# Kernel optimization log

Measured on AMD Instinct MI355X. Metric: run time of the kernel, lower is better.

## Reference

```python
import jax, jax.numpy as jnp
import numpy as np
import math

D_MODEL = 1024
NHEAD = 16
SEQ_LEN = 4096
K_PROJ = 16
HEAD_DIM = D_MODEL // NHEAD


def setup_inputs() -> dict:
    key = jax.random.key(0)
    ks = jax.random.split(key, 11)
    x = jax.random.normal(ks[0], (4, SEQ_LEN, D_MODEL), dtype=jnp.float32)
    s = 1.0 / math.sqrt(D_MODEL)
    Wq = jax.random.uniform(ks[1], (D_MODEL, D_MODEL), minval=-s, maxval=s)
    bq = jax.random.uniform(ks[2], (D_MODEL,), minval=-s, maxval=s)
    Wk = jax.random.uniform(ks[3], (D_MODEL, D_MODEL), minval=-s, maxval=s)
    bk = jax.random.uniform(ks[4], (D_MODEL,), minval=-s, maxval=s)
    Wv = jax.random.uniform(ks[5], (D_MODEL, D_MODEL), minval=-s, maxval=s)
    bv = jax.random.uniform(ks[6], (D_MODEL,), minval=-s, maxval=s)
    Wo = jax.random.uniform(ks[7], (D_MODEL, D_MODEL), minval=-s, maxval=s)
    bo = jax.random.uniform(ks[8], (D_MODEL,), minval=-s, maxval=s)
    E = jax.random.normal(ks[9], (NHEAD, K_PROJ, SEQ_LEN)) * 0.02
    F = jax.random.normal(ks[10], (NHEAD, K_PROJ, SEQ_LEN)) * 0.02
    return {"x": x, "Wq": Wq, "bq": bq, "Wk": Wk, "bk": bk,
            "Wv": Wv, "bv": bv, "Wo": Wo, "bo": bo, "E": E, "F": F}


def reference(x, Wq, bq, Wk, bk, Wv, bv, Wo, bo, E, F):
    B, N, D = x.shape
    # torch Linear: y = x @ W.T + b
    q = x @ Wq.T + bq
    k = x @ Wk.T + bk
    v = x @ Wv.T + bv
    # [B, H, N, Dh]
    def split_heads(t):
        return t.reshape(B, N, NHEAD, HEAD_DIM).transpose(0, 2, 1, 3)
    q, k, v = split_heads(q), split_heads(k), split_heads(v)
    # low-rank projections of K, V along sequence: [B, H, Kp, Dh]
    k_lin = jnp.einsum('bhnd,hkn->bhkd', k, E)
    v_lin = jnp.einsum('bhnd,hkn->bhkd', v, F)
    scores = jnp.einsum('bhnd,bhkd->bhnk', q, k_lin) / math.sqrt(HEAD_DIM)
    attn = jax.nn.softmax(scores, axis=-1)  # dropout is identity in eval
    out = jnp.einsum('bhnk,bhkd->bhnd', attn, v_lin)
    out = out.transpose(0, 2, 1, 3).reshape(B, N, D)
    return out @ Wo.T + bo
```

## Files before the change

### kernel.cpp

```cpp
#include <hip/hip_runtime.h>
#include <hip/hip_bf16.h>

#define SEQLEN 4096

typedef __bf16 bf16x8 __attribute__((ext_vector_type(8)));
typedef float f32x4 __attribute__((ext_vector_type(4)));
typedef __attribute__((ext_vector_type(8))) unsigned short u16x8;

__device__ inline float bf2f(unsigned short s) {
  union { unsigned u; float f; } t; t.u = ((unsigned)s) << 16; return t.f;
}
__device__ inline unsigned short f2bf(float f) {
  __hip_bfloat16 h = __float2bfloat16(f);
  return *reinterpret_cast<unsigned short*>(&h);
}

__device__ inline void gload_lds16(const void* g, void* l) {
  __builtin_amdgcn_global_load_lds(
      (const __attribute__((address_space(1))) unsigned int*)g,
      (__attribute__((address_space(3))) unsigned int*)l, 16, 0, 0);
}

__global__ void cvt_f32_to_bf16(const float* __restrict__ s,
                                unsigned short* __restrict__ d, int n4) {
  int i = blockIdx.x * 256 + threadIdx.x;
  if (i >= n4) return;
  float4 v = reinterpret_cast<const float4*>(s)[i];
  ushort4 o;
  o.x = f2bf(v.x); o.y = f2bf(v.y); o.z = f2bf(v.z); o.w = f2bf(v.w);
  reinterpret_cast<ushort4*>(d)[i] = o;
}

__global__ void pack_bias(const float* __restrict__ a, const float* __restrict__ b,
                          const float* __restrict__ c, float* __restrict__ dst) {
  int i = blockIdx.x * 256 + threadIdx.x;
  if (i < 1024) { dst[i] = a[i]; dst[1024 + i] = b[i]; dst[2048 + i] = c[i]; }
}

template <typename OUT_T>
__global__ void gemm_bt(const unsigned short* __restrict__ A,
                        const unsigned short* __restrict__ B,
                        const float* __restrict__ bias, OUT_T* __restrict__ C,
                        int M, int N, int K, int ldc) {
  __shared__ __align__(16) unsigned short As[128 * 64];
  __shared__ __align__(16) unsigned short Bs[128 * 64];
  const int tid = threadIdx.x;
  const int lane = tid & 63, wv = tid >> 6;
  const int wr = wv >> 1, wc = wv & 1;
  const int r16 = lane & 15, kg = lane >> 4;
  const int brow = blockIdx.y * 128, bcol = blockIdx.x * 128;

  f32x4 acc[4][4];
#pragma unroll
  for (int m = 0; m < 4; ++m)
#pragma unroll
    for (int n = 0; n < 4; ++n) acc[m][n] = (f32x4)0.0f;

  for (int k0 = 0; k0 < K; k0 += 64) {
#pragma unroll
    for (int it = 0; it < 4; ++it) {
      int f = it * 256 + tid;
      int row = f >> 3, ch = f & 7;
      const unsigned short* ga = A + (size_t)(brow + row) * K + k0 + ch * 8;
      const unsigned short* gb = B + (size_t)(bcol + row) * K + k0 + ch * 8;
      gload_lds16(ga, &As[f * 8]);
      gload_lds16(gb, &Bs[f * 8]);
    }
    __syncthreads();
#pragma unroll
    for (int ks = 0; ks < 2; ++ks) {
      bf16x8 a[4], b[4];
#pragma unroll
      for (int m = 0; m < 4; ++m)
        a[m] = *reinterpret_cast<const bf16x8*>(
            &As[(wr * 64 + m * 16 + r16) * 64 + ks * 32 + kg * 8]);
#pragma unroll
      for (int n = 0; n < 4; ++n)
        b[n] = *reinterpret_cast<const bf16x8*>(
            &Bs[(wc * 64 + n * 16 + r16) * 64 + ks * 32 + kg * 8]);
#pragma unroll
      for (int m = 0; m < 4; ++m)
#pragma unroll
        for (int n = 0; n < 4; ++n)
          acc[m][n] =
              __builtin_amdgcn_mfma_f32_16x16x32_bf16(a[m], b[n], acc[m][n], 0, 0, 0);
    }
    __syncthreads();
  }

#pragma unroll
  for (int n = 0; n < 4; ++n) {
    int col = bcol + wc * 64 + n * 16 + r16;
    float bv = bias ? bias[col] : 0.0f;
#pragma unroll
    for (int m = 0; m < 4; ++m) {
#pragma unroll
      for (int r = 0; r < 4; ++r) {
        int row = brow + wr * 64 + m * 16 + kg * 4 + r;
        float v = acc[m][n][r] + bv;
        if constexpr (sizeof(OUT_T) == 2) {
          C[(size_t)row * ldc + col] = f2bf(v);
        } else {
          C[(size_t)row * ldc + col] = v;
        }
      }
    }
  }
}

__global__ void kvlin_part(const unsigned short* __restrict__ qkv,
                           const float* __restrict__ E, const float* __restrict__ F,
                           float* __restrict__ part) {
  __shared__ __align__(16) unsigned short Ks[128 * 64], Vs[128 * 64];
  __shared__ __align__(16) float Es[16 * 128], Fs[16 * 128];
  const int tid = threadIdx.x;
  const int bid = blockIdx.x;
  const int bh = bid >> 3, ns = bid & 7;
  const int b = bh >> 4, h = bh & 15;
  const int d = tid & 63, kk = tid >> 6;
  float aK[4] = {0, 0, 0, 0}, aV[4] = {0, 0, 0, 0};
  for (int c = 0; c < 4; ++c) {
    int n0 = ns * 512 + c * 128;
#pragma unroll
    for (int it = 0; it < 4; ++it) {
      int f = it * 256 + tid;
      int row = f >> 3, ch = f & 7;
      const unsigned short* gk =
          qkv + (size_t)(b * SEQLEN + n0 + row) * 3072 + 1024 + h * 64 + ch * 8;
      gload_lds16(gk, &Ks[f * 8]);
      gload_lds16(gk + 1024, &Vs[f * 8]);
    }
#pragma unroll
    for (int it = 0; it < 2; ++it) {
      int f = it * 256 + tid;
      int k = f >> 5, ch = f & 31;
      const float* ge = E + (size_t)(h * 16 + k) * SEQLEN + n0 + ch * 4;
      const float* gf = F + (size_t)(h * 16 + k) * SEQLEN + n0 + ch * 4;
      gload_lds16(ge, &Es[f * 4]);
      gload_lds16(gf, &Fs[f * 4]);
    }
    __syncthreads();
    for (int n = 0; n < 128; ++n) {
      float kv = bf2f(Ks[n * 64 + d]);
      float vv = bf2f(Vs[n * 64 + d]);
#pragma unroll
      for (int j = 0; j < 4; ++j) {
        aK[j] += Es[(kk * 4 + j) * 128 + n] * kv;
        aV[j] += Fs[(kk * 4 + j) * 128 + n] * vv;
      }
    }
    __syncthreads();
  }
  size_t base = ((size_t)ns * 64 + bh) * 2048;
#pragma unroll
  for (int j = 0; j < 4; ++j) {
    part[base + (kk * 4 + j) * 64 + d] = aK[j];
    part[base + 1024 + (kk * 4 + j) * 64 + d] = aV[j];
  }
}

__global__ void kvlin_reduce(const float* __restrict__ part, float* __restrict__ out) {
  int i = blockIdx.x * 256 + threadIdx.x;
  float s = 0;
#pragma unroll
  for (int ns = 0; ns < 8; ++ns) s += part[(size_t)ns * 131072 + i];
  out[i] = s;
}

__global__ void attn_kernel(const unsigned short* __restrict__ qkv,
                            const float* __restrict__ kvlin,
                            unsigned short* __restrict__ aout) {
  __shared__ float kl[1024], vl[1024];
  const int tid = threadIdx.x;
  const int bid = blockIdx.x;
  const int bh = bid >> 4, nt = bid & 15;
  const int b = bh >> 4, h = bh & 15;
  for (int i = tid; i < 1024; i += 256) {
    kl[i] = kvlin[(size_t)bh * 2048 + i];
    vl[i] = kvlin[(size_t)bh * 2048 + 1024 + i];
  }
  __syncthreads();
  const int n = nt * 256 + tid;
  const unsigned short* qp = qkv + (size_t)(b * SEQLEN + n) * 3072 + h * 64;
  float q[64];
#pragma unroll
  for (int c2 = 0; c2 < 8; ++c2) {
    u16x8 v = *reinterpret_cast<const u16x8*>(qp + c2 * 8);
#pragma unroll
    for (int j = 0; j < 8; ++j) q[c2 * 8 + j] = bf2f(v[j]);
  }
  float s[16];
#pragma unroll
  for (int k = 0; k < 16; ++k) {
    float a = 0;
#pragma unroll
    for (int dd = 0; dd < 64; ++dd) a += q[dd] * kl[k * 64 + dd];
    s[k] = a * 0.125f;
  }
  float mx = s[0];
#pragma unroll
  for (int k = 1; k < 16; ++k) mx = fmaxf(mx, s[k]);
  float sum = 0;
#pragma unroll
  for (int k = 0; k < 16; ++k) { s[k] = __expf(s[k] - mx); sum += s[k]; }
  float inv = 1.0f / sum;
#pragma unroll
  for (int k = 0; k < 16; ++k) s[k] *= inv;
  unsigned short* op = aout + (size_t)(b * SEQLEN + n) * 1024 + h * 64;
#pragma unroll
  for (int d0 = 0; d0 < 8; ++d0) {
    float o[8] = {0, 0, 0, 0, 0, 0, 0, 0};
#pragma unroll
    for (int k = 0; k < 16; ++k) {
      float p = s[k];
#pragma unroll
      for (int j = 0; j < 8; ++j) o[j] += p * vl[k * 64 + d0 * 8 + j];
    }
    u16x8 pk;
#pragma unroll
    for (int j = 0; j < 8; ++j) pk[j] = f2bf(o[j]);
    *reinterpret_cast<u16x8*>(op + d0 * 8) = pk;
  }
}

extern "C" void kernel_launch(void* const* d_in, const int* in_sizes, int n_in,
                              void* d_out, int out_size, void* d_ws, size_t ws_size,
                              hipStream_t stream) {
  const float* x  = (const float*)d_in[0];
  const float* Wq = (const float*)d_in[1];
  const float* bq = (const float*)d_in[2];
  const float* Wk = (const float*)d_in[3];
  const float* bk = (const float*)d_in[4];
  const float* Wv = (const float*)d_in[5];
  const float* bv = (const float*)d_in[6];
  const float* Wo = (const float*)d_in[7];
  const float* bo = (const float*)d_in[8];
  const float* E  = (const float*)d_in[9];
  const float* F  = (const float*)d_in[10];
  float* out = (float*)d_out;

  char* ws = (char*)d_ws;
  unsigned short* Xb   = (unsigned short*)(ws);
  unsigned short* Wqkv = (unsigned short*)(ws + 33554432);
  unsigned short* WoB  = (unsigned short*)(ws + 39845888);
  float*          Bqkv = (float*)(ws + 41943040);
  unsigned short* QKV  = (unsigned short*)(ws + 41955328);
  float*          KVp  = (float*)(ws + 142618624);
  float*          KVl  = (float*)(ws + 146812928);
  unsigned short* AOut = Xb;

  cvt_f32_to_bf16<<<16384, 256, 0, stream>>>(x, Xb, 4194304);
  cvt_f32_to_bf16<<<1024, 256, 0, stream>>>(Wq, Wqkv, 262144);
  cvt_f32_to_bf16<<<1024, 256, 0, stream>>>(Wk, Wqkv + 1048576, 262144);
  cvt_f32_to_bf16<<<1024, 256, 0, stream>>>(Wv, Wqkv + 2097152, 262144);
  cvt_f32_to_bf16<<<1024, 256, 0, stream>>>(Wo, WoB, 262144);
  pack_bias<<<4, 256, 0, stream>>>(bq, bk, bv, Bqkv);

  gemm_bt<unsigned short><<<dim3(24, 128), 256, 0, stream>>>(
      Xb, Wqkv, Bqkv, QKV, 16384, 3072, 1024, 3072);

  kvlin_part<<<512, 256, 0, stream>>>(QKV, E, F, KVp);
  kvlin_reduce<<<512, 256, 0, stream>>>(KVp, KVl);
  attn_kernel<<<1024, 256, 0, stream>>>(QKV, KVl, AOut);

  gemm_bt<float><<<dim3(8, 128), 256, 0, stream>>>(
      AOut, WoB, bo, out, 16384, 1024, 1024, 1024);
}
```

Measured before the change: 281.8 us.

## Rewrite GEMM as 256x256 double-buffered 8-wave kernel with swizzled LDS

Replaces the 128x128 single-buffered GEMM with a 256x256 tile, 512-thread kernel that double-buffers A/B tiles in 128KB of dynamic LDS. Global-to-LDS loads for the next k-tile are interleaved with MFMA phases, using explicit vmcnt waits and barriers, and s_setprio raises priority around the MFMA blocks. LDS columns are XOR-swizzled to avoid bank conflicts, and the block order is remapped for L2 locality. The aim is to hide memory latency and raise arithmetic intensity in both projection GEMMs. The cost is higher register pressure and reliance on hand-tuned wait counts.

New measurement: 275.8 us. 1.02x faster.

```diff
diff --git a/kernel.cpp b/kernel.cpp
--- a/kernel.cpp
+++ b/kernel.cpp
@@ -37,66 +37,130 @@
   if (i < 1024) { dst[i] = a[i]; dst[1024 + i] = b[i]; dst[2048 + i] = c[i]; }
 }
 
+
+#define MFMA16(mk, A00, A01, A10, A11)                                          \
+  __builtin_amdgcn_s_setprio(1);                                                \
+  _Pragma("unroll")                                                             \
+  for (int n = 0; n < 4; ++n) {                                                 \
+    acc[2*(mk)][n]   = __builtin_amdgcn_mfma_f32_16x16x32_bf16(A00, b[n][0], acc[2*(mk)][n],   0, 0, 0); \
+    acc[2*(mk)][n]   = __builtin_amdgcn_mfma_f32_16x16x32_bf16(A01, b[n][1], acc[2*(mk)][n],   0, 0, 0); \
+    acc[2*(mk)+1][n] = __builtin_amdgcn_mfma_f32_16x16x32_bf16(A10, b[n][0], acc[2*(mk)+1][n], 0, 0, 0); \
+    acc[2*(mk)+1][n] = __builtin_amdgcn_mfma_f32_16x16x32_bf16(A11, b[n][1], acc[2*(mk)+1][n], 0, 0, 0); \
+  }                                                                             \
+  __builtin_amdgcn_s_setprio(0);
+
+#define LDA8(mi, sg) (*reinterpret_cast<const bf16x8*>(&as[((wr << 7) + (mi) * 16 + r16) * 64 + (sg) * 8]))
+#define LDB8(ni, sg) (*reinterpret_cast<const bf16x8*>(&bs[((wc << 6) + (ni) * 16 + r16) * 64 + (sg) * 8]))
+
 template <typename OUT_T>
-__global__ void gemm_bt(const unsigned short* __restrict__ A,
-                        const unsigned short* __restrict__ B,
-                        const float* __restrict__ bias, OUT_T* __restrict__ C,
-                        int M, int N, int K, int ldc) {
-  __shared__ __align__(16) unsigned short As[128 * 64];
-  __shared__ __align__(16) unsigned short Bs[128 * 64];
+__global__ __launch_bounds__(512, 2) void gemm8p(
+    const unsigned short* __restrict__ A, const unsigned short* __restrict__ B,
+    const float* __restrict__ bias, OUT_T* __restrict__ C, int M, int N, int K,
+    int ldc) {
+  extern __shared__ __align__(16) unsigned short lds[];
+
   const int tid = threadIdx.x;
   const int lane = tid & 63, wv = tid >> 6;
-  const int wr = wv >> 1, wc = wv & 1;
+  const int wr = wv >> 2, wc = wv & 3;
   const int r16 = lane & 15, kg = lane >> 4;
-  const int brow = blockIdx.y * 128, bcol = blockIdx.x * 128;
-
-  f32x4 acc[4][4];
-#pragma unroll
-  for (int m = 0; m < 4; ++m)
+  const int sg0 = (0 * 4 + kg) ^ (r16 & 7);
+  const int sg1 = (1 * 4 + kg) ^ (r16 & 7);
+
+  const int nwg = gridDim.x;
+  const int cpx = nwg >> 3;
+  const int swz = ((int)blockIdx.x & 7) * cpx + ((int)blockIdx.x >> 3);
+  const int mt = M >> 8;
+  const int tile_m = swz % mt, tile_n = swz / mt;
+  const int brow = tile_m << 8, bcol = tile_n << 8;
+
+  const unsigned short* Ag = A + (size_t)brow * K;
+  const unsigned short* Bg = B + (size_t)bcol * K;
+
+  const int sr = tid >> 3;
+  const int sc = tid & 7;
+  const int sgl = sc ^ (sr & 7);
+
+  auto STG = [&](const unsigned short* G, unsigned short* dstbuf, int row0, int kt) {
+    gload_lds16(G + (size_t)(row0 + sr) * K + (size_t)kt * 64 + sgl * 8,
+                dstbuf + (row0 + sr) * 64 + sc * 8);
+  };
+
+  f32x4 acc[8][4];
+#pragma unroll
+  for (int m = 0; m < 8; ++m)
 #pragma unroll
     for (int n = 0; n < 4; ++n) acc[m][n] = (f32x4)0.0f;
 
-  for (int k0 = 0; k0 < K; k0 += 64) {
-#pragma unroll
-    for (int it = 0; it < 4; ++it) {
-      int f = it * 256 + tid;
-      int row = f >> 3, ch = f & 7;
-      const unsigned short* ga = A + (size_t)(brow + row) * K + k0 + ch * 8;
-      const unsigned short* gb = B + (size_t)(bcol + row) * K + k0 + ch * 8;
-      gload_lds16(ga, &As[f * 8]);
-      gload_lds16(gb, &Bs[f * 8]);
-    }
-    __syncthreads();
-#pragma unroll
-    for (int ks = 0; ks < 2; ++ks) {
-      bf16x8 a[4], b[4];
-#pragma unroll
-      for (int m = 0; m < 4; ++m)
-        a[m] = *reinterpret_cast<const bf16x8*>(
-            &As[(wr * 64 + m * 16 + r16) * 64 + ks * 32 + kg * 8]);
-#pragma unroll
-      for (int n = 0; n < 4; ++n)
-        b[n] = *reinterpret_cast<const bf16x8*>(
-            &Bs[(wc * 64 + n * 16 + r16) * 64 + ks * 32 + kg * 8]);
-#pragma unroll
-      for (int m = 0; m < 4; ++m)
-#pragma unroll
-        for (int n = 0; n < 4; ++n)
-          acc[m][n] =
-              __builtin_amdgcn_mfma_f32_16x16x32_bf16(a[m], b[n], acc[m][n], 0, 0, 0);
-    }
-    __syncthreads();
-  }
+  {
+    unsigned short* a0 = lds;
+    unsigned short* b0 = lds + 32768;
+    STG(Ag, a0, 0, 0);   STG(Ag, a0, 128, 0);
+    STG(Bg, b0, 0, 0);   STG(Bg, b0, 64, 0);
+    STG(Bg, b0, 128, 0); STG(Bg, b0, 192, 0);
+    STG(Ag, a0, 64, 0);  STG(Ag, a0, 192, 0);
+  }
+  asm volatile("s_waitcnt vmcnt(2)" ::: "memory");
+  __builtin_amdgcn_s_barrier();
+
+  const int NT = K >> 6;
+  for (int t = 0; t < NT; ++t) {
+    const int cur = t & 1;
+    const unsigned short* as = lds + (cur << 14);
+    const unsigned short* bs = lds + 32768 + (cur << 14);
+    unsigned short* an = lds + ((cur ^ 1) << 14);
+    unsigned short* bn = lds + 32768 + ((cur ^ 1) << 14);
+    const int tn = (t + 1 < NT) ? t + 1 : 0;
+
+    bf16x8 b[4][2];
+#pragma unroll
+    for (int n = 0; n < 4; ++n) { b[n][0] = LDB8(n, sg0); b[n][1] = LDB8(n, sg1); }
+
+    {
+      bf16x8 a00 = LDA8(0, sg0), a01 = LDA8(0, sg1);
+      bf16x8 a10 = LDA8(1, sg0), a11 = LDA8(1, sg1);
+      STG(Ag, an, 0, tn); STG(Ag, an, 128, tn);
+      __builtin_amdgcn_s_barrier();
+      MFMA16(0, a00, a01, a10, a11);
+      __builtin_amdgcn_s_barrier();
+    }
+    {
+      bf16x8 a00 = LDA8(2, sg0), a01 = LDA8(2, sg1);
+      bf16x8 a10 = LDA8(3, sg0), a11 = LDA8(3, sg1);
+      STG(Bg, bn, 0, tn); STG(Bg, bn, 64, tn);
+      __builtin_amdgcn_s_barrier();
+      MFMA16(1, a00, a01, a10, a11);
+      asm volatile("s_waitcnt vmcnt(4)" ::: "memory");
+      __builtin_amdgcn_s_barrier();
+    }
+    {
+      bf16x8 a00 = LDA8(4, sg0), a01 = LDA8(4, sg1);
+      bf16x8 a10 = LDA8(5, sg0), a11 = LDA8(5, sg1);
+      STG(Bg, bn, 128, tn); STG(Bg, bn, 192, tn);
+      __builtin_amdgcn_s_barrier();
+      MFMA16(2, a00, a01, a10, a11);
+      __builtin_amdgcn_s_barrier();
+    }
+    {
+      bf16x8 a00 = LDA8(6, sg0), a01 = LDA8(6, sg1);
+      bf16x8 a10 = LDA8(7, sg0), a11 = LDA8(7, sg1);
+      STG(Ag, an, 64, tn); STG(Ag, an, 192, tn);
+      __builtin_amdgcn_s_barrier();
+      MFMA16(3, a00, a01, a10, a11);
+      asm volatile("s_waitcnt vmcnt(2)" ::: "memory");
+      __builtin_amdgcn_s_barrier();
+    }
+  }
+  asm volatile("s_waitcnt vmcnt(0)" ::: "memory");
 
 #pragma unroll
   for (int n = 0; n < 4; ++n) {
     int col = bcol + wc * 64 + n * 16 + r16;
     float bv = bias ? bias[col] : 0.0f;
 #pragma unroll
-    for (int m = 0; m < 4; ++m) {
+    for (int m = 0; m < 8; ++m) {
 #pragma unroll
       for (int r = 0; r < 4; ++r) {
-        int row = brow + wr * 64 + m * 16 + kg * 4 + r;
+        int row = brow + wr * 128 + m * 16 + kg * 4 + r;
         float v = acc[m][n][r] + bv;
         if constexpr (sizeof(OUT_T) == 2) {
           C[(size_t)row * ldc + col] = f2bf(v);
@@ -249,6 +313,11 @@
   float*          KVl  = (float*)(ws + 146812928);
   unsigned short* AOut = Xb;
 
+  (void)hipFuncSetAttribute(reinterpret_cast<const void*>(gemm8p<unsigned short>),
+                            hipFuncAttributeMaxDynamicSharedMemorySize, 131072);
+  (void)hipFuncSetAttribute(reinterpret_cast<const void*>(gemm8p<float>),
+                            hipFuncAttributeMaxDynamicSharedMemorySize, 131072);
+
   cvt_f32_to_bf16<<<16384, 256, 0, stream>>>(x, Xb, 4194304);
   cvt_f32_to_bf16<<<1024, 256, 0, stream>>>(Wq, Wqkv, 262144);
   cvt_f32_to_bf16<<<1024, 256, 0, stream>>>(Wk, Wqkv + 1048576, 262144);
@@ -256,13 +325,13 @@
   cvt_f32_to_bf16<<<1024, 256, 0, stream>>>(Wo, WoB, 262144);
   pack_bias<<<4, 256, 0, stream>>>(bq, bk, bv, Bqkv);
 
-  gemm_bt<unsigned short><<<dim3(24, 128), 256, 0, stream>>>(
+  gemm8p<unsigned short><<<768, 512, 131072, stream>>>(
       Xb, Wqkv, Bqkv, QKV, 16384, 3072, 1024, 3072);
 
   kvlin_part<<<512, 256, 0, stream>>>(QKV, E, F, KVp);
   kvlin_reduce<<<512, 256, 0, stream>>>(KVp, KVl);
   attn_kernel<<<1024, 256, 0, stream>>>(QKV, KVl, AOut);
 
-  gemm_bt<float><<<dim3(8, 128), 256, 0, stream>>>(
+  gemm8p<float><<<256, 512, 131072, stream>>>(
       AOut, WoB, bo, out, 16384, 1024, 1024, 1024);
 }
```
